# Optimization experiments

Measured on AMD Instinct MI355X. Metric: run time of the kernel, lower is better.

## Reference

```python
import jax, jax.numpy as jnp
import numpy as np

MAX_ITER = 10   # float32 branch of cg()
TOL = 1e-10

def _cdot(a, b):
    # complex_dot: sum(conj(a) * b) over all elements
    return jnp.sum(jnp.conj(a) * b)

def _A(p, smaps, mask):
    # p: [H,W] complex, smaps: [C,H,W] complex, mask: [H,W] real
    return jnp.fft.fft2(smaps * p[None], norm='ortho') * mask[None]

def _AH(y, smaps, mask):
    imgs = jnp.fft.ifft2(y * mask[None], norm='ortho')
    return jnp.sum(jnp.conj(smaps) * imgs, axis=0)  # [H,W]

def _cg(M, rhs):
    # conjugate gradient, faithful to the TF while_loop body
    def cond(s):
        i, rTr, x, r, p = s
        return jnp.logical_and(i < MAX_ITER, rTr > TOL)
    def body(s):
        i, rTr, x, r, p = s
        Ap = M(p)
        alpha = rTr / jnp.real(_cdot(p, Ap))
        x = x + p * alpha
        r = r - Ap * alpha
        rTrNew = jnp.real(_cdot(r, r))
        beta = rTrNew / rTr
        p = r + p * beta
        return (i + 1, rTrNew, x, r, p)
    rTr0 = jnp.real(_cdot(rhs, rhs))
    s0 = (jnp.int32(0), rTr0, jnp.zeros_like(rhs), rhs, rhs)
    return jax.lax.while_loop(cond, body, s0)[2]

def _solve_one(lambdaa, rhs, smaps, mask):
    M = lambda p: _AH(_A(p, smaps, mask), smaps, mask) + p * lambdaa
    return _cg(M, rhs)

_solve_b = jax.vmap(_solve_one, in_axes=(None, 0, 0, 0))  # replaces map_fn
_AH_b = jax.vmap(_AH, in_axes=(0, 0, 0))

def setup_inputs():
    key = jax.random.key(0)
    ks = jax.random.split(key, 7)
    B, C, H, W = 4, 16, 384, 384
    f = lambda k, s: jax.random.normal(k, s, dtype=jnp.float32)
    return {
        'lambdaa': 0.05 * jnp.ones((), jnp.float32),
        'x_re': f(ks[0], (B, H, W)),
        'x_im': f(ks[1], (B, H, W)),
        'y_re': f(ks[2], (B, C, H, W)),
        'y_im': f(ks[3], (B, C, H, W)),
        'smaps_re': f(ks[4], (B, C, H, W)),
        'smaps_im': f(ks[5], (B, C, H, W)),
        'mask': (jax.random.uniform(ks[6], (B, H, W)) < 0.33).astype(jnp.float32),
    }

def reference(lambdaa, x_re, x_im, y_re, y_im, smaps_re, smaps_im, mask):
    x = jax.lax.complex(x_re, x_im)
    y = jax.lax.complex(y_re, y_im)
    smaps = jax.lax.complex(smaps_re, smaps_im)
    # rhs = AH(y) + lambdaa * x
    rhs = _AH_b(y, smaps, mask) + x * lambdaa
    out = _solve_b(lambdaa, rhs, smaps, mask)  # [B,H,W] complex
    return jnp.stack([out.real, out.imag], axis=-1)  # [B,H,W,2] float32
```

## Files before the change

### kernel.cpp

```cpp
#include <hip/hip_runtime.h>


#define Bn 4
#define Cn 16
#define Hn 384
#define Wn 384
#define NPIX (Hn*Wn)
#define TPB 256
#define CTPB 512
#define NCOL 16
#define TOLF 1e-10f
#define NITER 10
#define RED_BLKS 72
#define RPITCH 416
#define CPITCH 417

__device__ __forceinline__ float2 cadd(float2 a, float2 b){ return make_float2(a.x+b.x, a.y+b.y); }
__device__ __forceinline__ float2 csub(float2 a, float2 b){ return make_float2(a.x-b.x, a.y-b.y); }
__device__ __forceinline__ float2 cmulf(float2 a, float2 b){
  return make_float2(a.x*b.x - a.y*b.y, a.x*b.y + a.y*b.x);
}

__device__ __forceinline__ void wave_fence(){ asm volatile("s_waitcnt lgkmcnt(0)" ::: "memory"); }

template<int IMM>
__device__ __forceinline__ float2 shx(float2 v){
  int x = __builtin_amdgcn_ds_swizzle(__float_as_int(v.x), IMM);
  int y = __builtin_amdgcn_ds_swizzle(__float_as_int(v.y), IMM);
  return make_float2(__int_as_float(x), __int_as_float(y));
}

__device__ __forceinline__ int rev5(int x){
  return ((x&1)<<4) | ((x&2)<<2) | (x&4) | ((x&8)>>2) | ((x&16)>>4);
}

__device__ __forceinline__ int offmap(int w){ return w + ((w*683)>>13); }

template<int DIR>
__device__ __forceinline__ void fft12(float2* v)
{
  const float S3 = (DIR<0) ? -0.86602540378443864676f : 0.86602540378443864676f;
  const float sg = (DIR<0) ? -1.f : 1.f;
  float2 t[4][3];
#pragma unroll
  for (int b = 0; b < 4; ++b) {
    float2 a0 = v[b], a1 = v[4+b], a2 = v[8+b];
    float2 s = cadd(a1,a2), d = csub(a1,a2);
    float2 mm = make_float2(a0.x - 0.5f*s.x, a0.y - 0.5f*s.y);
    float2 e  = make_float2(-d.y*S3, d.x*S3);
    t[b][0] = cadd(a0,s);
    t[b][1] = cadd(mm,e);
    t[b][2] = csub(mm,e);
  }
  const float2 w1  = make_float2(0.86602540378443864676f, sg*0.5f);
  const float2 w2  = make_float2(0.5f, sg*0.86602540378443864676f);
  const float2 w3  = make_float2(0.f, sg);
  const float2 w4t = make_float2(-0.5f, sg*0.86602540378443864676f);
  const float2 w6  = make_float2(-1.f, 0.f);
  t[1][1] = cmulf(t[1][1], w1);  t[1][2] = cmulf(t[1][2], w2);
  t[2][1] = cmulf(t[2][1], w2);  t[2][2] = cmulf(t[2][2], w4t);
  t[3][1] = cmulf(t[3][1], w3);  t[3][2] = cmulf(t[3][2], w6);
#pragma unroll
  for (int c = 0; c < 3; ++c) {
    float2 e = cadd(t[0][c], t[2][c]);
    float2 f = csub(t[0][c], t[2][c]);
    float2 g = cadd(t[1][c], t[3][c]);
    float2 h = csub(t[1][c], t[3][c]);
    float2 ih = (DIR<0) ? make_float2(h.y, -h.x) : make_float2(-h.y, h.x);
    v[c]   = cadd(e,g);
    v[c+3] = cadd(f,ih);
    v[c+6] = csub(e,g);
    v[c+9] = csub(f,ih);
  }
}

template<int DIR>
__device__ __forceinline__ void fft32_lanes(float2* v, int li)
{
  const float c2pi = (DIR<0) ? -6.2831853071795864769f : 6.2831853071795864769f;
  const float sg   = (DIR<0) ? -1.f : 1.f;
  float s, c;
  __sincosf(c2pi*(1.f/32.f)*(float)(li&15), &s, &c); float2 wA = make_float2(c,s);
  __sincosf(c2pi*(1.f/16.f)*(float)(li&7),  &s, &c); float2 wB = make_float2(c,s);
  __sincosf(c2pi*(1.f/ 8.f)*(float)(li&3),  &s, &c); float2 wC = make_float2(c,s);
  bool bA = li & 16, bB = li & 8, bC = li & 4, bD = li & 2, bE = li & 1;
#pragma unroll
  for (int k = 0; k < 12; ++k) {
    float2 a = v[k], o;
    o = shx<0x401F>(a); a = bA ? cmulf(csub(o,a), wA) : cadd(a,o);
    o = shx<0x201F>(a); a = bB ? cmulf(csub(o,a), wB) : cadd(a,o);
    o = shx<0x101F>(a); a = bC ? cmulf(csub(o,a), wC) : cadd(a,o);
    o = shx<0x081F>(a);
    { float2 su = cadd(a,o), d = csub(o,a);
      float2 dw = bE ? make_float2(-sg*d.y, sg*d.x) : d;
      a = bD ? dw : su; }
    o = shx<0x041F>(a); a = bE ? csub(o,a) : cadd(a,o);
    v[k] = a;
  }
}

template<int DIR>
__device__ __forceinline__ void fft384(float2* v, int li)
{
  fft12<DIR>(v);
  const float c2pi = (DIR<0) ? -6.2831853071795864769f : 6.2831853071795864769f;
  float s, c;
  __sincosf(c2pi*(1.f/384.f)*(float)li, &s, &c);
  float2 W = make_float2(c,s), cw = W;
#pragma unroll
  for (int k = 1; k < 12; ++k) { v[k] = cmulf(v[k], cw); cw = cmulf(cw, W); }
  fft32_lanes<DIR>(v, li);
}


__global__ __launch_bounds__(TPB) void k_row_fwd(
    const float2* __restrict__ p, const float* __restrict__ Sre,
    const float* __restrict__ Sim, float2* __restrict__ tmp)
{
  __shared__ float2 lbuf[8*RPITCH];
  int tid = threadIdx.x;
  int wave = tid>>6, lane = tid&63, sub = lane>>5, li = lane&31;
  int row = wave*2 + sub;
  int tile = blockIdx.x % (Hn/8);
  int bc   = blockIdx.x / (Hn/8);
  int b = bc / Cn;
  int h = tile*8 + row;
  size_t gbase = (size_t)bc*NPIX + (size_t)h*Wn;
  size_t pbase = (size_t)b*NPIX + (size_t)h*Wn;

  float2 v[12];
#pragma unroll
  for (int k = 0; k < 12; ++k) {
    int w = 32*k + li;
    float2 pv = p[pbase + w];
    float sr = Sre[gbase + w], si = Sim[gbase + w];
    v[k] = make_float2(sr*pv.x - si*pv.y, sr*pv.y + si*pv.x);
  }
  fft384<-1>(v, li);
  int m = rev5(li);
  float2* lrow = lbuf + row*RPITCH;
#pragma unroll
  for (int k = 0; k < 12; ++k) lrow[13*m + k] = v[k];
  wave_fence();
#pragma unroll
  for (int k = 0; k < 12; ++k) {
    int w = 32*k + li;
    tmp[gbase + w] = lrow[offmap(w)];
  }
}

template<int CPGt>
__global__ __launch_bounds__(TPB) void k_row_inv_acc(
    const float2* __restrict__ tmp, const float* __restrict__ Sre,
    const float* __restrict__ Sim, float2* __restrict__ partial)
{
  const int GRPt = Cn/CPGt;
  __shared__ float2 lbuf[8*RPITCH];
  int tid = threadIdx.x;
  int wave = tid>>6, lane = tid&63, sub = lane>>5, li = lane&31;
  int row = wave*2 + sub;
  int tile = blockIdx.x % (Hn/8);
  int rest = blockIdx.x / (Hn/8);
  int g = rest % GRPt;
  int b = rest / GRPt;
  int h = tile*8 + row;
  int m = rev5(li);
  float2* lrow = lbuf + row*RPITCH;

  float2 acc[12];
#pragma unroll
  for (int k = 0; k < 12; ++k) acc[k] = make_float2(0.f, 0.f);

  for (int j = 0; j < CPGt; ++j) {
    size_t bc = (size_t)b*Cn + (g*CPGt + j);
    size_t gbase = bc*NPIX + (size_t)h*Wn;
    float2 v[12];
#pragma unroll
    for (int k = 0; k < 12; ++k) v[k] = tmp[gbase + 32*k + li];
    fft384<1>(v, li);
    wave_fence();
#pragma unroll
    for (int k = 0; k < 12; ++k) lrow[13*m + k] = v[k];
    wave_fence();
#pragma unroll
    for (int k = 0; k < 12; ++k) {
      int w = 32*k + li;
      float2 u = lrow[offmap(w)];
      float sr = Sre[gbase + w], si = Sim[gbase + w];
      acc[k].x += sr*u.x + si*u.y;
      acc[k].y += sr*u.y - si*u.x;
    }
  }
  size_t pbase = ((size_t)g*Bn + b)*NPIX + (size_t)h*Wn;
#pragma unroll
  for (int k = 0; k < 12; ++k) partial[pbase + 32*k + li] = acc[k];
}

__global__ __launch_bounds__(TPB) void k_maskp(
    const float* __restrict__ mask, float* __restrict__ maskP)
{
  int idx = blockIdx.x*TPB + threadIdx.x;
  if (idx >= Bn*NPIX) return;
  int k = idx % 12; int t = idx / 12;
  int li = t & 31; t >>= 5;
  int w = t % Wn;  int b = t / Wn;
  maskP[idx] = mask[((size_t)b*Hn + (k + 12*rev5(li)))*Wn + w] * (1.0f/(float)NPIX);
}

__global__ __launch_bounds__(CTPB) void k_col_full(
    float2* __restrict__ tmp, const float* __restrict__ maskP)
{
  __shared__ float2 dbuf[NCOL*CPITCH];
  int tid = threadIdx.x;
  int wave = tid>>6, lane = tid&63, sub = lane>>5, li = lane&31;
  int col = wave*2 + sub;
  int tile = blockIdx.x % (Wn/NCOL);
  int bc   = blockIdx.x / (Wn/NCOL);
  int b = bc / Cn;
  int w0 = tile*NCOL;
  size_t tbase = (size_t)bc*NPIX;

  for (int e = tid; e < NCOL*Hn; e += CTPB) {
    int wi = e & (NCOL-1), h = e >> 4;
    dbuf[wi*CPITCH + offmap(h)] = tmp[tbase + (size_t)h*Wn + w0 + wi];
  }
  __syncthreads();

  float2* drow = dbuf + col*CPITCH;
  int w = w0 + col;
  int m = rev5(li);
  float2 v[12];
#pragma unroll
  for (int k = 0; k < 12; ++k) v[k] = drow[offmap(32*k + li)];
  fft384<-1>(v, li);
  const float4* mp4 = (const float4*)(maskP + (((size_t)b*Wn + w)*32 + li)*12);
  float4 m0 = mp4[0], m1 = mp4[1], m2 = mp4[2];
  float mk[12] = {m0.x,m0.y,m0.z,m0.w, m1.x,m1.y,m1.z,m1.w, m2.x,m2.y,m2.z,m2.w};
#pragma unroll
  for (int k = 0; k < 12; ++k) v[k] = make_float2(v[k].x*mk[k], v[k].y*mk[k]);
  wave_fence();
#pragma unroll
  for (int k = 0; k < 12; ++k) drow[13*m + k] = v[k];
  wave_fence();
#pragma unroll
  for (int k = 0; k < 12; ++k) v[k] = drow[offmap(32*k + li)];
  fft384<1>(v, li);
  wave_fence();
#pragma unroll
  for (int k = 0; k < 12; ++k) drow[13*m + k] = v[k];
  __syncthreads();

  for (int e = tid; e < NCOL*Hn; e += CTPB) {
    int wi = e & (NCOL-1), h = e >> 4;
    tmp[tbase + (size_t)h*Wn + w0 + wi] = dbuf[wi*CPITCH + offmap(h)];
  }
}

__global__ __launch_bounds__(CTPB) void k_col_rhs(
    const float* __restrict__ yre, const float* __restrict__ yim,
    const float* __restrict__ mask, float2* __restrict__ tmp)
{
  __shared__ float2 dbuf[NCOL*CPITCH];
  int tid = threadIdx.x;
  int wave = tid>>6, lane = tid&63, sub = lane>>5, li = lane&31;
  int col = wave*2 + sub;
  int tile = blockIdx.x % (Wn/NCOL);
  int bc   = blockIdx.x / (Wn/NCOL);
  int b = bc / Cn;
  int w0 = tile*NCOL;
  size_t tbase = (size_t)bc*NPIX;
  size_t mbase = (size_t)b*NPIX;

  for (int e = tid; e < NCOL*Hn; e += CTPB) {
    int wi = e & (NCOL-1), h = e >> 4;
    size_t gi = (size_t)h*Wn + w0 + wi;
    float mv = mask[mbase + gi] * (1.0f/384.0f);
    dbuf[wi*CPITCH + offmap(h)] = make_float2(yre[tbase+gi]*mv, yim[tbase+gi]*mv);
  }
  __syncthreads();

  float2* drow = dbuf + col*CPITCH;
  int m = rev5(li);
  float2 v[12];
#pragma unroll
  for (int k = 0; k < 12; ++k) v[k] = drow[offmap(32*k + li)];
  fft384<1>(v, li);
  wave_fence();
#pragma unroll
  for (int k = 0; k < 12; ++k) drow[13*m + k] = v[k];
  __syncthreads();

  for (int e = tid; e < NCOL*Hn; e += CTPB) {
    int wi = e & (NCOL-1), h = e >> 4;
    tmp[tbase + (size_t)h*Wn + w0 + wi] = dbuf[wi*CPITCH + offmap(h)];
  }
}


__global__ void k_zero_scal(float* __restrict__ scal)
{
  int i = threadIdx.x;
  if (i < 96) scal[i] = 0.0f;
}

__device__ __forceinline__ void block_reduce_atomic(float sum, float* target)
{
  __shared__ float red[TPB];
  red[threadIdx.x] = sum; __syncthreads();
  for (int s = TPB/2; s > 0; s >>= 1) {
    if (threadIdx.x < s) red[threadIdx.x] += red[threadIdx.x + s];
    __syncthreads();
  }
  if (threadIdx.x == 0) unsafeAtomicAdd(target, red[0]);
}

template<int GRPt>
__global__ __launch_bounds__(TPB) void k_rhs_init(
    const float* __restrict__ xre, const float* __restrict__ xim,
    const float* __restrict__ lam, const float2* __restrict__ partial,
    float2* __restrict__ r, float2* __restrict__ p, float2* __restrict__ x,
    float* __restrict__ scal)
{
  int b = blockIdx.y;
  float l = lam[0];
  float sum = 0.0f;
  for (int i = blockIdx.x*TPB + threadIdx.x; i < NPIX; i += RED_BLKS*TPB) {
    size_t gi = (size_t)b*NPIX + i;
    float2 rv = make_float2(l*xre[gi], l*xim[gi]);
#pragma unroll
    for (int g = 0; g < GRPt; ++g) {
      float2 pv = partial[((size_t)g*Bn + b)*NPIX + i];
      rv.x += pv.x; rv.y += pv.y;
    }
    r[gi] = rv; p[gi] = rv;
    x[gi] = make_float2(0.0f, 0.0f);
    sum += rv.x*rv.x + rv.y*rv.y;
  }
  block_reduce_atomic(sum, &scal[b]);
}

template<int GRPt>
__global__ __launch_bounds__(TPB) void k_combine_dot(
    const float2* __restrict__ p, const float* __restrict__ lam,
    const float2* __restrict__ partial, float2* __restrict__ Ap,
    float* __restrict__ slot)
{
  int b = blockIdx.y;
  float l = lam[0];
  float sum = 0.0f;
  for (int i = blockIdx.x*TPB + threadIdx.x; i < NPIX; i += RED_BLKS*TPB) {
    size_t gi = (size_t)b*NPIX + i;
    float2 pv = p[gi];
    float2 av = make_float2(l*pv.x, l*pv.y);
#pragma unroll
    for (int g = 0; g < GRPt; ++g) {
      float2 qv = partial[((size_t)g*Bn + b)*NPIX + i];
      av.x += qv.x; av.y += qv.y;
    }
    Ap[gi] = av;
    sum += pv.x*av.x + pv.y*av.y;
  }
  block_reduce_atomic(sum, &slot[b]);
}

__global__ __launch_bounds__(TPB) void k_upd1(
    float2* __restrict__ x, float2* __restrict__ r,
    const float2* __restrict__ p, const float2* __restrict__ Ap,
    const float* __restrict__ rtr_cur, float* __restrict__ rtr_new,
    const float* __restrict__ pap)
{
  int b = blockIdx.y;
  float rtr = rtr_cur[b];
  bool act = rtr > TOLF;
  float alpha = act ? rtr / pap[b] : 0.0f;
  float sum = 0.0f;
  for (int i = blockIdx.x*TPB + threadIdx.x; i < NPIX; i += RED_BLKS*TPB) {
    size_t gi = (size_t)b*NPIX + i;
    float2 rv = r[gi];
    if (act) {
      float2 pv = p[gi], av = Ap[gi], xv = x[gi];
      xv.x += alpha*pv.x; xv.y += alpha*pv.y;
      rv.x -= alpha*av.x; rv.y -= alpha*av.y;
      x[gi] = xv; r[gi] = rv;
    }
    sum += rv.x*rv.x + rv.y*rv.y;
  }
  block_reduce_atomic(sum, &rtr_new[b]);
}

__global__ __launch_bounds__(TPB) void k_upd2(
    float2* __restrict__ p, const float2* __restrict__ r,
    const float* __restrict__ rtr_cur, const float* __restrict__ rtr_new)
{
  int b = blockIdx.y;
  float rtr = rtr_cur[b];
  if (!(rtr > TOLF)) return;
  float beta = rtr_new[b] / rtr;
  for (int i = blockIdx.x*TPB + threadIdx.x; i < NPIX; i += RED_BLKS*TPB) {
    size_t gi = (size_t)b*NPIX + i;
    float2 rv = r[gi];
    float2 pv = p[gi];
    p[gi] = make_float2(rv.x + beta*pv.x, rv.y + beta*pv.y);
  }
}


extern "C" void kernel_launch(void* const* d_in, const int* in_sizes, int n_in,
                              void* d_out, int out_size, void* d_ws, size_t ws_size,
                              hipStream_t stream)
{
  const float* lam  = (const float*)d_in[0];
  const float* xre  = (const float*)d_in[1];
  const float* xim  = (const float*)d_in[2];
  const float* yre  = (const float*)d_in[3];
  const float* yim  = (const float*)d_in[4];
  const float* sre  = (const float*)d_in[5];
  const float* sim  = (const float*)d_in[6];
  const float* mask = (const float*)d_in[7];

  const size_t szTmp  = (size_t)Bn*Cn*NPIX*sizeof(float2);
  const size_t szVec  = (size_t)Bn*NPIX*sizeof(float2);
  const size_t szMask = (size_t)Bn*NPIX*sizeof(float);
  const size_t need8  = szTmp + 8*szVec + 3*szVec + 512 + szMask;
  const int GRP = (ws_size >= need8) ? 8 : 4;

  char* ws = (char*)d_ws;
  float2* tmp  = (float2*)ws;  ws += szTmp;
  float2* part = (float2*)ws;  ws += (size_t)GRP*szVec;
  float2* r    = (float2*)ws;  ws += szVec;
  float2* p    = (float2*)ws;  ws += szVec;
  float2* Ap   = (float2*)ws;  ws += szVec;
  float*  scal = (float*)ws;   ws += 512;
  float*  mskP = (float*)ws;
  float2* x    = (float2*)d_out;

  dim3 blk(TPB);
  dim3 rg(RED_BLKS, Bn);
  int grid_row = Bn*Cn*(Hn/8);
  int grid_col = Bn*Cn*(Wn/NCOL);
  int grid_inv = Bn*GRP*(Hn/8);

  k_zero_scal<<<1, 128, 0, stream>>>(scal);
  k_maskp<<<(Bn*NPIX + TPB-1)/TPB, blk, 0, stream>>>(mask, mskP);

  k_col_rhs<<<grid_col, CTPB, 0, stream>>>(yre, yim, mask, tmp);
  if (GRP == 8) {
    k_row_inv_acc<2><<<grid_inv, blk, 0, stream>>>(tmp, sre, sim, part);
    k_rhs_init<8><<<rg, blk, 0, stream>>>(xre, xim, lam, part, r, p, x, scal);
  } else {
    k_row_inv_acc<4><<<grid_inv, blk, 0, stream>>>(tmp, sre, sim, part);
    k_rhs_init<4><<<rg, blk, 0, stream>>>(xre, xim, lam, part, r, p, x, scal);
  }

  for (int it = 0; it < NITER; ++it) {
    k_row_fwd<<<grid_row, blk, 0, stream>>>(p, sre, sim, tmp);
    k_col_full<<<grid_col, CTPB, 0, stream>>>(tmp, mskP);
    if (GRP == 8) {
      k_row_inv_acc<2><<<grid_inv, blk, 0, stream>>>(tmp, sre, sim, part);
      k_combine_dot<8><<<rg, blk, 0, stream>>>(p, lam, part, Ap, scal + 44 + it*Bn);
    } else {
      k_row_inv_acc<4><<<grid_inv, blk, 0, stream>>>(tmp, sre, sim, part);
      k_combine_dot<4><<<rg, blk, 0, stream>>>(p, lam, part, Ap, scal + 44 + it*Bn);
    }
    k_upd1<<<rg, blk, 0, stream>>>(x, r, p, Ap, scal + it*Bn, scal + (it+1)*Bn, scal + 44 + it*Bn);
    if (it < NITER-1)
      k_upd2<<<rg, blk, 0, stream>>>(p, r, scal + it*Bn, scal + (it+1)*Bn);
  }
}
```

Before: 1.635 ms.

## Vectorize column transposes and CG vector kernels, prefetch rows, fuse scalar zeroing

Column FFT kernels switch to 12-column tiles with 384 threads and use float4 global loads and stores for the transpose in and out of shared memory. The row inverse-FFT accumulation kernel prefetches the next coil's row into registers while the current one is transformed. The CG elementwise kernels (init, combine-dot, updates) process two complex values per thread with float4 accesses. The scalar-zeroing kernel is folded into the mask permutation kernel to save a launch. These changes target memory-access efficiency and launch overhead, at the cost of more registers for the prefetch and a different tile shape for the column kernels.

```diff
diff --git a/kernel.cpp b/kernel.cpp
--- a/kernel.cpp
+++ b/kernel.cpp
@@ -7,8 +7,8 @@
 #define Wn 384
 #define NPIX (Hn*Wn)
 #define TPB 256
-#define CTPB 512
-#define NCOL 16
+#define CTPB 384
+#define NCOL 12
 #define TOLF 1e-10f
 #define NITER 10
 #define RED_BLKS 72
@@ -167,29 +167,39 @@
   int m = rev5(li);
   float2* lrow = lbuf + row*RPITCH;
 
+  size_t gbase0 = ((size_t)b*Cn + g*CPGt)*NPIX + (size_t)h*Wn;
+  float2 vc[12], vn[12];
+#pragma unroll
+  for (int k = 0; k < 12; ++k) vc[k] = tmp[gbase0 + 32*k + li];
+
   float2 acc[12];
 #pragma unroll
   for (int k = 0; k < 12; ++k) acc[k] = make_float2(0.f, 0.f);
 
   for (int j = 0; j < CPGt; ++j) {
-    size_t bc = (size_t)b*Cn + (g*CPGt + j);
-    size_t gbase = bc*NPIX + (size_t)h*Wn;
-    float2 v[12];
-#pragma unroll
-    for (int k = 0; k < 12; ++k) v[k] = tmp[gbase + 32*k + li];
-    fft384<1>(v, li);
+    size_t gb = gbase0 + (size_t)j*NPIX;
+    if (j + 1 < CPGt) {
+      size_t gbn = gb + NPIX;
+#pragma unroll
+      for (int k = 0; k < 12; ++k) vn[k] = tmp[gbn + 32*k + li];
+    }
+    fft384<1>(vc, li);
     wave_fence();
 #pragma unroll
-    for (int k = 0; k < 12; ++k) lrow[13*m + k] = v[k];
+    for (int k = 0; k < 12; ++k) lrow[13*m + k] = vc[k];
     wave_fence();
 #pragma unroll
     for (int k = 0; k < 12; ++k) {
       int w = 32*k + li;
       float2 u = lrow[offmap(w)];
-      float sr = Sre[gbase + w], si = Sim[gbase + w];
+      float sr = Sre[gb + w], si = Sim[gb + w];
       acc[k].x += sr*u.x + si*u.y;
       acc[k].y += sr*u.y - si*u.x;
     }
+    if (j + 1 < CPGt) {
+#pragma unroll
+      for (int k = 0; k < 12; ++k) vc[k] = vn[k];
+    }
   }
   size_t pbase = ((size_t)g*Bn + b)*NPIX + (size_t)h*Wn;
 #pragma unroll
@@ -197,9 +207,11 @@
 }
 
 __global__ __launch_bounds__(TPB) void k_maskp(
-    const float* __restrict__ mask, float* __restrict__ maskP)
+    const float* __restrict__ mask, float* __restrict__ maskP,
+    float* __restrict__ scal)
 {
   int idx = blockIdx.x*TPB + threadIdx.x;
+  if (blockIdx.x == 0 && threadIdx.x < 96) scal[threadIdx.x] = 0.0f;
   if (idx >= Bn*NPIX) return;
   int k = idx % 12; int t = idx / 12;
   int li = t & 31; t >>= 5;
@@ -220,21 +232,26 @@
   int w0 = tile*NCOL;
   size_t tbase = (size_t)bc*NPIX;
 
-  for (int e = tid; e < NCOL*Hn; e += CTPB) {
-    int wi = e & (NCOL-1), h = e >> 4;
-    dbuf[wi*CPITCH + offmap(h)] = tmp[tbase + (size_t)h*Wn + w0 + wi];
+#pragma unroll
+  for (int t = 0; t < 6; ++t) {
+    int pi = tid + CTPB*t;
+    int h = pi / 6, wp = pi - 6*h;
+    float4 q = *(const float4*)(tmp + tbase + (size_t)h*Wn + w0 + 2*wp);
+    int off = offmap(h);
+    dbuf[(2*wp  )*CPITCH + off] = make_float2(q.x, q.y);
+    dbuf[(2*wp+1)*CPITCH + off] = make_float2(q.z, q.w);
   }
   __syncthreads();
 
   float2* drow = dbuf + col*CPITCH;
   int w = w0 + col;
   int m = rev5(li);
+  const float4* mp4 = (const float4*)(maskP + (((size_t)b*Wn + w)*32 + li)*12);
+  float4 m0 = mp4[0], m1 = mp4[1], m2 = mp4[2];
   float2 v[12];
 #pragma unroll
   for (int k = 0; k < 12; ++k) v[k] = drow[offmap(32*k + li)];
   fft384<-1>(v, li);
-  const float4* mp4 = (const float4*)(maskP + (((size_t)b*Wn + w)*32 + li)*12);
-  float4 m0 = mp4[0], m1 = mp4[1], m2 = mp4[2];
   float mk[12] = {m0.x,m0.y,m0.z,m0.w, m1.x,m1.y,m1.z,m1.w, m2.x,m2.y,m2.z,m2.w};
 #pragma unroll
   for (int k = 0; k < 12; ++k) v[k] = make_float2(v[k].x*mk[k], v[k].y*mk[k]);
@@ -250,9 +267,14 @@
   for (int k = 0; k < 12; ++k) drow[13*m + k] = v[k];
   __syncthreads();
 
-  for (int e = tid; e < NCOL*Hn; e += CTPB) {
-    int wi = e & (NCOL-1), h = e >> 4;
-    tmp[tbase + (size_t)h*Wn + w0 + wi] = dbuf[wi*CPITCH + offmap(h)];
+#pragma unroll
+  for (int t = 0; t < 6; ++t) {
+    int pi = tid + CTPB*t;
+    int h = pi / 6, wp = pi - 6*h;
+    int off = offmap(h);
+    float2 a = dbuf[(2*wp  )*CPITCH + off];
+    float2 bq = dbuf[(2*wp+1)*CPITCH + off];
+    *(float4*)(tmp + tbase + (size_t)h*Wn + w0 + 2*wp) = make_float4(a.x, a.y, bq.x, bq.y);
   }
 }
 
@@ -271,11 +293,20 @@
   size_t tbase = (size_t)bc*NPIX;
   size_t mbase = (size_t)b*NPIX;
 
-  for (int e = tid; e < NCOL*Hn; e += CTPB) {
-    int wi = e & (NCOL-1), h = e >> 4;
-    size_t gi = (size_t)h*Wn + w0 + wi;
-    float mv = mask[mbase + gi] * (1.0f/384.0f);
-    dbuf[wi*CPITCH + offmap(h)] = make_float2(yre[tbase+gi]*mv, yim[tbase+gi]*mv);
+#pragma unroll
+  for (int t = 0; t < 3; ++t) {
+    int qi = tid + CTPB*t;
+    int h = qi / 3, wq = qi - 3*h;
+    size_t gi = (size_t)h*Wn + w0 + 4*wq;
+    float4 re = *(const float4*)(yre + tbase + gi);
+    float4 im = *(const float4*)(yim + tbase + gi);
+    float4 mm = *(const float4*)(mask + mbase + gi);
+    int off = offmap(h);
+    const float SC = 1.0f/384.0f;
+    dbuf[(4*wq  )*CPITCH + off] = make_float2(re.x*mm.x*SC, im.x*mm.x*SC);
+    dbuf[(4*wq+1)*CPITCH + off] = make_float2(re.y*mm.y*SC, im.y*mm.y*SC);
+    dbuf[(4*wq+2)*CPITCH + off] = make_float2(re.z*mm.z*SC, im.z*mm.z*SC);
+    dbuf[(4*wq+3)*CPITCH + off] = make_float2(re.w*mm.w*SC, im.w*mm.w*SC);
   }
   __syncthreads();
 
@@ -290,18 +321,19 @@
   for (int k = 0; k < 12; ++k) drow[13*m + k] = v[k];
   __syncthreads();
 
-  for (int e = tid; e < NCOL*Hn; e += CTPB) {
-    int wi = e & (NCOL-1), h = e >> 4;
-    tmp[tbase + (size_t)h*Wn + w0 + wi] = dbuf[wi*CPITCH + offmap(h)];
-  }
-}
-
-
-__global__ void k_zero_scal(float* __restrict__ scal)
-{
-  int i = threadIdx.x;
-  if (i < 96) scal[i] = 0.0f;
-}
+#pragma unroll
+  for (int t = 0; t < 6; ++t) {
+    int pi = tid + CTPB*t;
+    int h = pi / 6, wp = pi - 6*h;
+    int off = offmap(h);
+    float2 a = dbuf[(2*wp  )*CPITCH + off];
+    float2 bq = dbuf[(2*wp+1)*CPITCH + off];
+    *(float4*)(tmp + tbase + (size_t)h*Wn + w0 + 2*wp) = make_float4(a.x, a.y, bq.x, bq.y);
+  }
+}
+
+
+#define NPIX2 (NPIX/2)
 
 __device__ __forceinline__ void block_reduce_atomic(float sum, float* target)
 {
@@ -324,17 +356,22 @@
   int b = blockIdx.y;
   float l = lam[0];
   float sum = 0.0f;
-  for (int i = blockIdx.x*TPB + threadIdx.x; i < NPIX; i += RED_BLKS*TPB) {
-    size_t gi = (size_t)b*NPIX + i;
-    float2 rv = make_float2(l*xre[gi], l*xim[gi]);
+  const float2* xr2 = (const float2*)(xre + (size_t)b*NPIX);
+  const float2* xi2 = (const float2*)(xim + (size_t)b*NPIX);
+  float4* r4 = (float4*)(r + (size_t)b*NPIX);
+  float4* p4 = (float4*)(p + (size_t)b*NPIX);
+  float4* x4 = (float4*)(x + (size_t)b*NPIX);
+  for (int i = blockIdx.x*TPB + threadIdx.x; i < NPIX2; i += RED_BLKS*TPB) {
+    float2 re = xr2[i], im = xi2[i];
+    float4 rv = make_float4(l*re.x, l*im.x, l*re.y, l*im.y);
 #pragma unroll
     for (int g = 0; g < GRPt; ++g) {
-      float2 pv = partial[((size_t)g*Bn + b)*NPIX + i];
-      rv.x += pv.x; rv.y += pv.y;
-    }
-    r[gi] = rv; p[gi] = rv;
-    x[gi] = make_float2(0.0f, 0.0f);
-    sum += rv.x*rv.x + rv.y*rv.y;
+      float4 pv = ((const float4*)(partial + ((size_t)g*Bn + b)*NPIX))[i];
+      rv.x += pv.x; rv.y += pv.y; rv.z += pv.z; rv.w += pv.w;
+    }
+    r4[i] = rv; p4[i] = rv;
+    x4[i] = make_float4(0.f, 0.f, 0.f, 0.f);
+    sum += rv.x*rv.x + rv.y*rv.y + rv.z*rv.z + rv.w*rv.w;
   }
   block_reduce_atomic(sum, &scal[b]);
 }
@@ -348,17 +385,18 @@
   int b = blockIdx.y;
   float l = lam[0];
   float sum = 0.0f;
-  for (int i = blockIdx.x*TPB + threadIdx.x; i < NPIX; i += RED_BLKS*TPB) {
-    size_t gi = (size_t)b*NPIX + i;
-    float2 pv = p[gi];
-    float2 av = make_float2(l*pv.x, l*pv.y);
+  const float4* p4 = (const float4*)(p + (size_t)b*NPIX);
+  float4* A4 = (float4*)(Ap + (size_t)b*NPIX);
+  for (int i = blockIdx.x*TPB + threadIdx.x; i < NPIX2; i += RED_BLKS*TPB) {
+    float4 pv = p4[i];
+    float4 av = make_float4(l*pv.x, l*pv.y, l*pv.z, l*pv.w);
 #pragma unroll
     for (int g = 0; g < GRPt; ++g) {
-      float2 qv = partial[((size_t)g*Bn + b)*NPIX + i];
-      av.x += qv.x; av.y += qv.y;
-    }
-    Ap[gi] = av;
-    sum += pv.x*av.x + pv.y*av.y;
+      float4 qv = ((const float4*)(partial + ((size_t)g*Bn + b)*NPIX))[i];
+      av.x += qv.x; av.y += qv.y; av.z += qv.z; av.w += qv.w;
+    }
+    A4[i] = av;
+    sum += pv.x*av.x + pv.y*av.y + pv.z*av.z + pv.w*av.w;
   }
   block_reduce_atomic(sum, &slot[b]);
 }
@@ -374,16 +412,19 @@
   bool act = rtr > TOLF;
   float alpha = act ? rtr / pap[b] : 0.0f;
   float sum = 0.0f;
-  for (int i = blockIdx.x*TPB + threadIdx.x; i < NPIX; i += RED_BLKS*TPB) {
-    size_t gi = (size_t)b*NPIX + i;
-    float2 rv = r[gi];
+  float4* x4 = (float4*)(x + (size_t)b*NPIX);
+  float4* r4 = (float4*)(r + (size_t)b*NPIX);
+  const float4* p4 = (const float4*)(p + (size_t)b*NPIX);
+  const float4* A4 = (const float4*)(Ap + (size_t)b*NPIX);
+  for (int i = blockIdx.x*TPB + threadIdx.x; i < NPIX2; i += RED_BLKS*TPB) {
+    float4 rv = r4[i];
     if (act) {
-      float2 pv = p[gi], av = Ap[gi], xv = x[gi];
-      xv.x += alpha*pv.x; xv.y += alpha*pv.y;
-      rv.x -= alpha*av.x; rv.y -= alpha*av.y;
-      x[gi] = xv; r[gi] = rv;
-    }
-    sum += rv.x*rv.x + rv.y*rv.y;
+      float4 pv = p4[i], av = A4[i], xv = x4[i];
+      xv.x += alpha*pv.x; xv.y += alpha*pv.y; xv.z += alpha*pv.z; xv.w += alpha*pv.w;
+      rv.x -= alpha*av.x; rv.y -= alpha*av.y; rv.z -= alpha*av.z; rv.w -= alpha*av.w;
+      x4[i] = xv; r4[i] = rv;
+    }
+    sum += rv.x*rv.x + rv.y*rv.y + rv.z*rv.z + rv.w*rv.w;
   }
   block_reduce_atomic(sum, &rtr_new[b]);
 }
@@ -396,11 +437,13 @@
   float rtr = rtr_cur[b];
   if (!(rtr > TOLF)) return;
   float beta = rtr_new[b] / rtr;
-  for (int i = blockIdx.x*TPB + threadIdx.x; i < NPIX; i += RED_BLKS*TPB) {
-    size_t gi = (size_t)b*NPIX + i;
-    float2 rv = r[gi];
-    float2 pv = p[gi];
-    p[gi] = make_float2(rv.x + beta*pv.x, rv.y + beta*pv.y);
+  float4* p4 = (float4*)(p + (size_t)b*NPIX);
+  const float4* r4 = (const float4*)(r + (size_t)b*NPIX);
+  for (int i = blockIdx.x*TPB + threadIdx.x; i < NPIX2; i += RED_BLKS*TPB) {
+    float4 rv = r4[i];
+    float4 pv = p4[i];
+    p4[i] = make_float4(rv.x + beta*pv.x, rv.y + beta*pv.y,
+                        rv.z + beta*pv.z, rv.w + beta*pv.w);
   }
 }
 
@@ -440,8 +483,7 @@
   int grid_col = Bn*Cn*(Wn/NCOL);
   int grid_inv = Bn*GRP*(Hn/8);
 
-  k_zero_scal<<<1, 128, 0, stream>>>(scal);
-  k_maskp<<<(Bn*NPIX + TPB-1)/TPB, blk, 0, stream>>>(mask, mskP);
+  k_maskp<<<(Bn*NPIX)/TPB, blk, 0, stream>>>(mask, mskP, scal);
 
   k_col_rhs<<<grid_col, CTPB, 0, stream>>>(yre, yim, mask, tmp);
   if (GRP == 8) {
```

Measured after the change: 1.868 ms. 1.14x slower.
